# Performance work log

Hardware: AMD Instinct MI355X
Metric: run time of the kernel (lower is better)

The kernel has to match this reference:

```python
import jax, jax.numpy as jnp
import numpy as np

DIM = 512
PDIM = 64
NUM_HEAD = 8
HEAD_DIM = DIM // NUM_HEAD
SCALE = HEAD_DIM ** -0.5
EPS = 1e-6


def setup_inputs() -> dict:
    key = jax.random.key(0)
    ks = jax.random.split(key, 8)
    B, N = 8, 2048
    x_token = jax.random.normal(ks[0], (B, N, DIM), dtype=jnp.float32)
    x_path = jax.random.normal(ks[1], (B, N, PDIM), dtype=jnp.float32)
    idx_cluster = jax.random.randint(ks[2], (B, N), 0, 16, dtype=jnp.int32)
    # weights stored as [in, out] (y = x @ W + b), matching torch Linear math
    Wqk = jax.random.normal(ks[3], (DIM, 2 * DIM), dtype=jnp.float32) * 0.02
    Wv = jax.random.normal(ks[4], (DIM, DIM), dtype=jnp.float32) * 0.02
    Wpv = jax.random.normal(ks[5], (PDIM, PDIM), dtype=jnp.float32) * 0.02
    Wproj = jax.random.normal(ks[6], (DIM, DIM), dtype=jnp.float32) * 0.02
    bproj = jax.random.normal(ks[7], (DIM,), dtype=jnp.float32) * 0.02
    return {"x_token": x_token, "x_path": x_path, "idx_cluster": idx_cluster,
            "cluster_num": 16, "Wqk": Wqk, "Wv": Wv, "Wpv": Wpv,
            "Wproj": Wproj, "bproj": bproj}


def reference(x_token, x_path, idx_cluster, cluster_num, Wqk, Wv, Wpv, Wproj, bproj):
    B, N, C = x_token.shape
    qk = x_token @ Wqk                      # [B,N,2C]
    q, k = qk[..., :C], qk[..., C:]
    v = x_token @ Wv                        # [B,N,C]
    pv = x_path @ Wpv                       # dead code in original; kept for fidelity

    idx_shuffle = jnp.argsort(idx_cluster, axis=1)          # [B,N]
    idx_restore = jnp.argsort(idx_shuffle, axis=1)

    v_s = jnp.take_along_axis(v, idx_shuffle[..., None], axis=1)
    pv_s = jnp.take_along_axis(pv, idx_shuffle[..., None], axis=1)  # unused (faithful)

    attn_map = jnp.einsum('bic,bjc->bij', q, k) * SCALE     # [B,N,N]

    # torch does two gathers, both with dim=1; the second index is constant along
    # rows, so attn2[b,i,j] = attn_map[b, idx_shuffle[b, idx_shuffle[b,j]], j]
    double = jnp.take_along_axis(idx_shuffle, idx_shuffle, axis=1)  # [B,N]
    col_vals = jnp.take_along_axis(jnp.swapaxes(attn_map, 1, 2), double[..., None], axis=2)[..., 0]  # [B,N]
    attn = jnp.broadcast_to(col_vals[:, None, :], (B, N, N))

    # contiguous per-cluster block mask in sorted order == equality of sorted ids
    s = jnp.sort(idx_cluster, axis=1)
    mask = (s[:, :, None] == s[:, None, :]) & (s[:, :, None] < cluster_num)

    attn = jnp.where(mask, attn, jnp.float32(-1e9))
    attn = jnp.exp(attn.astype(jnp.float32))
    attn = (attn + EPS / N) / (jnp.sum(attn, axis=-1, keepdims=True) + EPS)

    out = attn @ v_s                                         # [B,N,C]
    out = jnp.swapaxes(out, 1, 2).reshape(B, N, C)           # faithful layout scramble
    out = jnp.take_along_axis(out, idx_restore[..., None], axis=1)
    x_out = out @ Wproj + bproj
    return x_out, attn_map
```

## Files before the change

### kernel.cpp

```cpp
#include <hip/hip_runtime.h>
#include <hip/hip_bf16.h>

typedef __attribute__((ext_vector_type(8))) short short8;
typedef __attribute__((ext_vector_type(4))) float floatx4;

__device__ __forceinline__ unsigned short f2bfu(float f) {
    unsigned u = __float_as_uint(f);
    unsigned rounding = 0x7fffu + ((u >> 16) & 1u);
    return (unsigned short)((u + rounding) >> 16);
}
__device__ __forceinline__ float bfu2f(unsigned short u) {
    return __uint_as_float(((unsigned)u) << 16);
}

__device__ __forceinline__ void async_ld16(const void* g, void* l) {
    __builtin_amdgcn_global_load_lds(
        (const __attribute__((address_space(1))) void*)g,
        (__attribute__((address_space(3))) void*)l, 16, 0, 0);
}

#define B_  8
#define N_  2048
#define C_  512
#define NC_ 16
#define SL_ 8

__global__ __launch_bounds__(256) void cvt_x(const float4* __restrict__ x,
                                             unsigned short* __restrict__ xbf) {
    size_t i = (size_t)blockIdx.x * 256 + threadIdx.x;
    float4 f = x[i];
    unsigned short u0 = f2bfu(f.x), u1 = f2bfu(f.y), u2 = f2bfu(f.z), u3 = f2bfu(f.w);
    uint2 p;
    p.x = (unsigned)u0 | ((unsigned)u1 << 16);
    p.y = (unsigned)u2 | ((unsigned)u3 << 16);
    *(uint2*)(xbf + 4 * i) = p;
}

__global__ __launch_bounds__(256) void cvt_wqkv(const float* __restrict__ Wqk,
                                                const float* __restrict__ Wv,
                                                unsigned short* __restrict__ WT) {
    int id = blockIdx.x * 256 + threadIdx.x;
    int n = id >> 9, k = id & 511;
    float v = (n < 1024) ? Wqk[(size_t)k * 1024 + n] : Wv[(size_t)k * 512 + (n - 1024)];
    WT[id] = f2bfu(v);
}

__global__ __launch_bounds__(256) void sort_kernel(const int* __restrict__ idx_cluster,
                                                   int* __restrict__ shuf,
                                                   int* __restrict__ restore,
                                                   int* __restrict__ svals,
                                                   int* __restrict__ dbl,
                                                   int* __restrict__ cstart) {
    int b = blockIdx.x, t = threadIdx.x;
    __shared__ int vals[N_];
    __shared__ int seghist[256 * 17];
    __shared__ int cbase[NC_], ctot[NC_];
    __shared__ int shufs[N_];
    const int* src = idx_cluster + (size_t)b * N_;
    for (int j = t; j < N_; j += 256) vals[j] = src[j];
    for (int c = 0; c < NC_; ++c) seghist[t * 17 + c] = 0;
    __syncthreads();
    for (int i = 0; i < 8; ++i) {
        int c = vals[t * 8 + i];
        seghist[t * 17 + c]++;
    }
    __syncthreads();
    if (t < NC_) {
        int run = 0;
        for (int s = 0; s < 256; ++s) {
            int x = seghist[s * 17 + t];
            seghist[s * 17 + t] = run;
            run += x;
        }
        ctot[t] = run;
    }
    __syncthreads();
    if (t == 0) {
        int run = 0;
        for (int c = 0; c < NC_; ++c) {
            cbase[c] = run;
            cstart[b * 17 + c] = run;
            run += ctot[c];
        }
        cstart[b * 17 + NC_] = run;
    }
    __syncthreads();
    for (int i = 0; i < 8; ++i) {
        int p = t * 8 + i;
        int c = vals[p];
        int pos = cbase[c] + seghist[t * 17 + c];
        seghist[t * 17 + c]++;
        shufs[pos] = p;
    }
    __syncthreads();
    for (int j = t; j < N_; j += 256) {
        int sj = shufs[j];
        shuf[(size_t)b * N_ + j] = sj;
        svals[(size_t)b * N_ + j] = vals[sj];
        restore[(size_t)b * N_ + sj] = j;
        dbl[(size_t)b * N_ + j] = shufs[sj];
    }
}

template <int MODE>
__global__ __launch_bounds__(256) void gemm_bt(const unsigned short* __restrict__ A,
                                               const unsigned short* __restrict__ Bt,
                                               float* __restrict__ outF,
                                               unsigned short* __restrict__ outQ,
                                               unsigned short* __restrict__ outK,
                                               unsigned short* __restrict__ outV,
                                               const float* __restrict__ bias) {
    constexpr int K = 512;
    constexpr int NT = K / 64;
    int t = threadIdx.x;
    int lane = t & 63, wave = t >> 6;
    int wm = (wave & 1) * 64, wn = (wave >> 1) * 64;
    int m0 = blockIdx.y * 128, n0 = blockIdx.x * 128;
    if (MODE == 1) {
        size_t b = blockIdx.z;
        A += b * (size_t)N_ * 512;
        Bt += b * (size_t)N_ * 512;
        outF += b * (size_t)N_ * N_;
    }
    __shared__ __align__(16) unsigned short As[2][128 * 64];
    __shared__ __align__(16) unsigned short Bs[2][128 * 64];
    floatx4 acc[4][4] = {};
    int l15 = lane & 15, q4 = lane >> 4;
    int srow = lane >> 3, schk = lane & 7;
    int sgc = schk ^ srow;
    int xr = l15 & 7;

    auto stage = [&](int buf, int k0) {
#pragma unroll
        for (int i = 0; i < 4; ++i) {
            int cid = i * 4 + wave;
            int row = cid * 8 + srow;
            async_ld16(A + (size_t)(m0 + row) * 512 + k0 + sgc * 8, (char*)As[buf] + cid * 1024);
            async_ld16(Bt + (size_t)(n0 + row) * 512 + k0 + sgc * 8, (char*)Bs[buf] + cid * 1024);
        }
    };
    auto compute = [&](int buf) {
#pragma unroll
        for (int kk = 0; kk < 2; ++kk) {
            int csw = (((kk * 4 + q4) ^ xr) * 8);
            short8 af[4], bfr[4];
#pragma unroll
            for (int mi = 0; mi < 4; ++mi)
                af[mi] = *(const short8*)(&As[buf][(wm + mi * 16 + l15) * 64 + csw]);
#pragma unroll
            for (int ni = 0; ni < 4; ++ni)
                bfr[ni] = *(const short8*)(&Bs[buf][(wn + ni * 16 + l15) * 64 + csw]);
#pragma unroll
            for (int mi = 0; mi < 4; ++mi)
#pragma unroll
                for (int ni = 0; ni < 4; ++ni)
                    acc[mi][ni] = __builtin_amdgcn_mfma_f32_16x16x32_bf16(af[mi], bfr[ni], acc[mi][ni], 0, 0, 0);
        }
    };

    stage(0, 0);
    __syncthreads();
    for (int it = 1; it < NT; ++it) {
        stage(it & 1, it * 64);
        compute((it - 1) & 1);
        __syncthreads();
    }
    compute((NT - 1) & 1);

#pragma unroll
    for (int mi = 0; mi < 4; ++mi) {
#pragma unroll
        for (int ni = 0; ni < 4; ++ni) {
#pragma unroll
            for (int r = 0; r < 4; ++r) {
                int row = m0 + wm + mi * 16 + q4 * 4 + r;
                int col = n0 + wn + ni * 16 + l15;
                float v = acc[mi][ni][r];
                if (MODE == 0) {
                    unsigned short u = f2bfu(v);
                    if (col < 512)       outQ[(size_t)row * 512 + col] = u;
                    else if (col < 1024) outK[(size_t)row * 512 + col - 512] = u;
                    else                 outV[(size_t)row * 512 + col - 1024] = u;
                } else {
                    outF[(size_t)row * N_ + col] = v * 0.125f;
                }
            }
        }
    }
}

__global__ __launch_bounds__(256) void cluster_reduce2(const float* __restrict__ attn,
                                                       const int* __restrict__ shuf,
                                                       const int* __restrict__ dbl,
                                                       const int* __restrict__ cstart,
                                                       const unsigned short* __restrict__ vbf,
                                                       float* __restrict__ Opart,
                                                       float* __restrict__ Spart) {
    int c = blockIdx.x, b = blockIdx.y, sl = blockIdx.z, t = threadIdx.x;
    int start = cstart[b * 17 + c], end = cstart[b * 17 + c + 1];
    int n = end - start;
    int i0 = (n * sl) / SL_, i1 = (n * (sl + 1)) / SL_;
    int cnt = i1 - i0;
    __shared__ float e_lds[256];
    __shared__ int row_lds[256];
    if (t < cnt) {
        int j = start + i0 + t;
        int dj = dbl[(size_t)b * N_ + j];
        float e = expf(attn[(size_t)b * N_ * N_ + (size_t)dj * N_ + j]);
        e_lds[t] = e;
        row_lds[t] = shuf[(size_t)b * N_ + j];
    }
    __syncthreads();
    if (t == 0) {
        float s = 0.f;
        for (int i = 0; i < cnt; ++i) s += e_lds[i];
        Spart[(b * SL_ + sl) * NC_ + c] = s;
    }
    float a0 = 0.f, a1 = 0.f;
    for (int i = 0; i < cnt; ++i) {
        float e = e_lds[i];
        unsigned u = *(const unsigned*)(vbf + ((size_t)b * N_ + row_lds[i]) * 512 + 2 * t);
        a0 += e * bfu2f((unsigned short)u);
        a1 += e * bfu2f((unsigned short)(u >> 16));
    }
    float2 o; o.x = a0; o.y = a1;
    *(float2*)(Opart + (((size_t)(b * SL_ + sl) * NC_ + c) * 512 + 2 * t)) = o;
}

__global__ __launch_bounds__(256) void combine_O(const float* __restrict__ Opart,
                                                 const float* __restrict__ Spart,
                                                 float* __restrict__ Ot) {
    int c = blockIdx.x, b = blockIdx.y, t = threadIdx.x;
    float S = 0.f;
    for (int sl = 0; sl < SL_; ++sl) S += Spart[(b * SL_ + sl) * NC_ + c];
    float inv = S > 0.f ? 1.f / S : 0.f;
    float a0 = 0.f, a1 = 0.f;
    for (int sl = 0; sl < SL_; ++sl) {
        float2 o = *(const float2*)(Opart + (((size_t)(b * SL_ + sl) * NC_ + c) * 512 + 2 * t));
        a0 += o.x; a1 += o.y;
    }
    Ot[((size_t)b * 512 + 2 * t) * NC_ + c] = a0 * inv;
    Ot[((size_t)b * 512 + 2 * t + 1) * NC_ + c] = a1 * inv;
}

__global__ __launch_bounds__(256) void build_wg(const float* __restrict__ Wproj,
                                                const int* __restrict__ cstart,
                                                unsigned int* __restrict__ Wg) {
    int c = blockIdx.x;
    int bg = blockIdx.y;
    int b = bg >> 2, g = bg & 3;
    int t = threadIdx.x;
    int lo = cstart[b * 17 + c] - g * 512;
    int hi = cstart[b * 17 + c + 1] - g * 512;
    lo = lo < 0 ? 0 : lo;
    hi = hi > 512 ? 512 : hi;
    float a0 = 0.f, a1 = 0.f;
    for (int cd = lo; cd < hi; ++cd) {
        float2 w = *(const float2*)(Wproj + (size_t)cd * 512 + 2 * t);
        a0 += w.x; a1 += w.y;
    }
    Wg[(size_t)bg * NC_ * 256 + c * 256 + t] =
        (unsigned)f2bfu(a0) | ((unsigned)f2bfu(a1) << 16);
}

__global__ __launch_bounds__(256) void xout_kernel(const float* __restrict__ Ot,
                                                   const unsigned int* __restrict__ Wg,
                                                   const int* __restrict__ restore,
                                                   const float* __restrict__ bias,
                                                   float* __restrict__ xout) {
    int nb = blockIdx.x, b = blockIdx.y, t = threadIdx.x;
    int n0 = nb * 64;
    __shared__ int r_lds[64];
    if (t < 64) r_lds[t] = restore[(size_t)b * N_ + n0 + t];
    __syncthreads();
    float b0 = bias[2 * t], b1 = bias[2 * t + 1];
    const float* Otb = Ot + (size_t)b * 512 * NC_;
    for (int g = 0; g < 4; ++g) {
        const unsigned int* wg = Wg + (size_t)(b * 4 + g) * NC_ * 256 + t;
        float wx[NC_], wy[NC_];
#pragma unroll
        for (int c = 0; c < NC_; ++c) {
            unsigned u = wg[c * 256];
            wx[c] = bfu2f((unsigned short)u);
            wy[c] = bfu2f((unsigned short)(u >> 16));
        }
        for (int i = 0; i < 64; ++i) {
            int r = r_lds[i];
            if ((r & 3) != g) continue;
            int rq = r >> 2;
            const float4* op = (const float4*)(Otb + rq * NC_);
            float o[NC_];
            *(float4*)&o[0]  = op[0];
            *(float4*)&o[4]  = op[1];
            *(float4*)&o[8]  = op[2];
            *(float4*)&o[12] = op[3];
            float a0 = b0, a1 = b1;
#pragma unroll
            for (int c = 0; c < NC_; ++c) { a0 += o[c] * wx[c]; a1 += o[c] * wy[c]; }
            float2 res; res.x = a0; res.y = a1;
            *(float2*)(xout + ((size_t)b * N_ + n0 + i) * 512 + 2 * t) = res;
        }
    }
}

extern "C" void kernel_launch(void* const* d_in, const int* in_sizes, int n_in,
                              void* d_out, int out_size, void* d_ws, size_t ws_size,
                              hipStream_t stream) {
    const float* x_token = (const float*)d_in[0];
    const int* idx_cluster = (const int*)d_in[2];
    const float* Wqk = (const float*)d_in[4];
    const float* Wv = (const float*)d_in[5];
    const float* Wproj = (const float*)d_in[7];
    const float* bproj = (const float*)d_in[8];

    float* x_out = (float*)d_out;
    float* attn = x_out + (size_t)B_ * N_ * C_;

    char* ws = (char*)d_ws;
    size_t off = 0;
    auto alloc = [&](size_t bytes) {
        void* p = ws + off;
        off += (bytes + 255) & ~(size_t)255;
        return p;
    };
    unsigned short* WqkvT = (unsigned short*)alloc(1536 * 512 * 2);
    unsigned short* xbf = (unsigned short*)alloc((size_t)B_ * N_ * C_ * 2);
    unsigned short* qbf = (unsigned short*)alloc((size_t)B_ * N_ * C_ * 2);
    unsigned short* kbf = (unsigned short*)alloc((size_t)B_ * N_ * C_ * 2);
    unsigned short* vbf = (unsigned short*)alloc((size_t)B_ * N_ * C_ * 2);
    int* shuf = (int*)alloc((size_t)B_ * N_ * 4);
    int* restore = (int*)alloc((size_t)B_ * N_ * 4);
    int* svals = (int*)alloc((size_t)B_ * N_ * 4);
    int* dbl = (int*)alloc((size_t)B_ * N_ * 4);
    int* cstart = (int*)alloc(B_ * 17 * 4);
    float* Ot = (float*)alloc((size_t)B_ * 512 * NC_ * 4);
    float* Opart = (float*)alloc((size_t)B_ * SL_ * NC_ * 512 * 4);
    float* Spart = (float*)alloc((size_t)B_ * SL_ * NC_ * 4);
    unsigned int* Wg = (unsigned int*)alloc((size_t)B_ * 4 * NC_ * 256 * 4);

    cvt_x<<<dim3((B_ * N_ * C_) / (256 * 4)), dim3(256), 0, stream>>>((const float4*)x_token, xbf);
    cvt_wqkv<<<dim3((1536 * 512) / 256), dim3(256), 0, stream>>>(Wqk, Wv, WqkvT);

    sort_kernel<<<dim3(B_), dim3(256), 0, stream>>>(idx_cluster, shuf, restore, svals, dbl, cstart);

    build_wg<<<dim3(NC_, B_ * 4), dim3(256), 0, stream>>>(Wproj, cstart, Wg);

    gemm_bt<0><<<dim3(1536 / 128, 16384 / 128, 1), dim3(256), 0, stream>>>(
        xbf, WqkvT, nullptr, qbf, kbf, vbf, nullptr);

    gemm_bt<1><<<dim3(N_ / 128, N_ / 128, B_), dim3(256), 0, stream>>>(
        qbf, kbf, attn, nullptr, nullptr, nullptr, nullptr);

    cluster_reduce2<<<dim3(NC_, B_, SL_), dim3(256), 0, stream>>>(
        attn, shuf, dbl, cstart, vbf, Opart, Spart);

    combine_O<<<dim3(NC_, B_), dim3(256), 0, stream>>>(Opart, Spart, Ot);

    xout_kernel<<<dim3(N_ / 64, B_), dim3(256), 0, stream>>>(Ot, Wg, restore, bproj, x_out);
}
```

Baseline: 403.7 us.

## Shrink GEMM K-tile to 32 and add XCD-aware workgroup swizzle

Halves the K-step of the bf16 MFMA GEMM tile from 64 to 32, which shrinks LDS usage per block to allow more resident blocks, and reworks the LDS XOR swizzle to match the narrower rows. It also remaps the linear block id so that consecutive ids land on the same XCD group (lid&7 striding), aiming for better L2 locality across chiplets. The cost is twice as many K iterations and barriers per tile, with less MFMA work between syncs.

```diff
diff --git a/kernel.cpp b/kernel.cpp
--- a/kernel.cpp
+++ b/kernel.cpp
@@ -111,57 +111,65 @@
                                                unsigned short* __restrict__ outV,
                                                const float* __restrict__ bias) {
     constexpr int K = 512;
-    constexpr int NT = K / 64;
+    constexpr int NT = K / 32;
     int t = threadIdx.x;
     int lane = t & 63, wave = t >> 6;
     int wm = (wave & 1) * 64, wn = (wave >> 1) * 64;
-    int m0 = blockIdx.y * 128, n0 = blockIdx.x * 128;
+
+    int gx = gridDim.x, gy = gridDim.y;
+    int nwg = gx * gy * gridDim.z;
+    int lid = blockIdx.x + gx * (blockIdx.y + gy * blockIdx.z);
+    int swz = (lid & 7) * (nwg >> 3) + (lid >> 3);
+    int bx = swz % gx;
+    int rem = swz / gx;
+    int by = rem % gy;
+    int bz = rem / gy;
+
+    int m0 = by * 128, n0 = bx * 128;
     if (MODE == 1) {
-        size_t b = blockIdx.z;
+        size_t b = (size_t)bz;
         A += b * (size_t)N_ * 512;
         Bt += b * (size_t)N_ * 512;
         outF += b * (size_t)N_ * N_;
     }
-    __shared__ __align__(16) unsigned short As[2][128 * 64];
-    __shared__ __align__(16) unsigned short Bs[2][128 * 64];
+    __shared__ __align__(16) unsigned short As[2][128 * 32];
+    __shared__ __align__(16) unsigned short Bs[2][128 * 32];
     floatx4 acc[4][4] = {};
     int l15 = lane & 15, q4 = lane >> 4;
-    int srow = lane >> 3, schk = lane & 7;
-    int sgc = schk ^ srow;
-    int xr = l15 & 7;
+    int fc = (l15 >> 1) & 3;
+
+    int s_r = lane >> 2;
+    int s_c = (lane & 3) ^ ((lane >> 3) & 3);
 
     auto stage = [&](int buf, int k0) {
 #pragma unroll
-        for (int i = 0; i < 4; ++i) {
-            int cid = i * 4 + wave;
-            int row = cid * 8 + srow;
-            async_ld16(A + (size_t)(m0 + row) * 512 + k0 + sgc * 8, (char*)As[buf] + cid * 1024);
-            async_ld16(Bt + (size_t)(n0 + row) * 512 + k0 + sgc * 8, (char*)Bs[buf] + cid * 1024);
+        for (int i = 0; i < 2; ++i) {
+            int grp = wave + i * 4;
+            int row = grp * 16 + s_r;
+            async_ld16(A + (size_t)(m0 + row) * 512 + k0 + s_c * 8, (char*)As[buf] + grp * 1024);
+            async_ld16(Bt + (size_t)(n0 + row) * 512 + k0 + s_c * 8, (char*)Bs[buf] + grp * 1024);
         }
     };
     auto compute = [&](int buf) {
-#pragma unroll
-        for (int kk = 0; kk < 2; ++kk) {
-            int csw = (((kk * 4 + q4) ^ xr) * 8);
-            short8 af[4], bfr[4];
-#pragma unroll
-            for (int mi = 0; mi < 4; ++mi)
-                af[mi] = *(const short8*)(&As[buf][(wm + mi * 16 + l15) * 64 + csw]);
+        int cs = (q4 ^ fc) * 8;
+        short8 af[4], bfr[4];
+#pragma unroll
+        for (int mi = 0; mi < 4; ++mi)
+            af[mi] = *(const short8*)(&As[buf][(wm + mi * 16 + l15) * 32 + cs]);
+#pragma unroll
+        for (int ni = 0; ni < 4; ++ni)
+            bfr[ni] = *(const short8*)(&Bs[buf][(wn + ni * 16 + l15) * 32 + cs]);
+#pragma unroll
+        for (int mi = 0; mi < 4; ++mi)
 #pragma unroll
             for (int ni = 0; ni < 4; ++ni)
-                bfr[ni] = *(const short8*)(&Bs[buf][(wn + ni * 16 + l15) * 64 + csw]);
-#pragma unroll
-            for (int mi = 0; mi < 4; ++mi)
-#pragma unroll
-                for (int ni = 0; ni < 4; ++ni)
-                    acc[mi][ni] = __builtin_amdgcn_mfma_f32_16x16x32_bf16(af[mi], bfr[ni], acc[mi][ni], 0, 0, 0);
-        }
+                acc[mi][ni] = __builtin_amdgcn_mfma_f32_16x16x32_bf16(af[mi], bfr[ni], acc[mi][ni], 0, 0, 0);
     };
 
     stage(0, 0);
     __syncthreads();
     for (int it = 1; it < NT; ++it) {
-        stage(it & 1, it * 64);
+        stage(it & 1, it * 32);
         compute((it - 1) & 1);
         __syncthreads();
     }
```

After: 377.1 us. -6.6%, faster.

## Apply Wv after cluster reduction and swizzle GEMM tiles with single-buffered LDS

Applied to the files above, without the earlier changes.

Uses linearity to drop the V projection from the big GEMM. The cluster reduction now sums exp-weighted bf16 x rows, and a small new kernel multiplies the per-cluster sums by Wv in fp32. This removes a third of the QKV GEMM's output columns and the V buffer writes. The GEMM also gets a workgroup-id swizzle for cache locality and swaps the double-buffered LDS pipeline for a single buffer with two barriers per k-step. That swap may expose load latency.

```diff
diff --git a/kernel.cpp b/kernel.cpp
--- a/kernel.cpp
+++ b/kernel.cpp
@@ -36,13 +36,11 @@
     *(uint2*)(xbf + 4 * i) = p;
 }
 
-__global__ __launch_bounds__(256) void cvt_wqkv(const float* __restrict__ Wqk,
-                                                const float* __restrict__ Wv,
-                                                unsigned short* __restrict__ WT) {
+__global__ __launch_bounds__(256) void cvt_wqk(const float* __restrict__ Wqk,
+                                               unsigned short* __restrict__ WT) {
     int id = blockIdx.x * 256 + threadIdx.x;
     int n = id >> 9, k = id & 511;
-    float v = (n < 1024) ? Wqk[(size_t)k * 1024 + n] : Wv[(size_t)k * 512 + (n - 1024)];
-    WT[id] = f2bfu(v);
+    WT[id] = f2bfu(Wqk[(size_t)k * 1024 + n]);
 }
 
 __global__ __launch_bounds__(256) void sort_kernel(const int* __restrict__ idx_cluster,
@@ -107,66 +105,63 @@
                                                const unsigned short* __restrict__ Bt,
                                                float* __restrict__ outF,
                                                unsigned short* __restrict__ outQ,
-                                               unsigned short* __restrict__ outK,
-                                               unsigned short* __restrict__ outV,
-                                               const float* __restrict__ bias) {
+                                               unsigned short* __restrict__ outK) {
     constexpr int K = 512;
-    constexpr int NT = K / 64;
     int t = threadIdx.x;
     int lane = t & 63, wave = t >> 6;
     int wm = (wave & 1) * 64, wn = (wave >> 1) * 64;
-    int m0 = blockIdx.y * 128, n0 = blockIdx.x * 128;
+
+    int gx = gridDim.x, gy = gridDim.y;
+    int nwg = gx * gy * gridDim.z;
+    int lid = blockIdx.x + gx * (blockIdx.y + gy * blockIdx.z);
+    int swz = (lid & 7) * (nwg >> 3) + (lid >> 3);
+    int bx = swz % gx;
+    int rem = swz / gx;
+    int by = rem % gy;
+    int bz = rem / gy;
+
+    int m0 = by * 128, n0 = bx * 128;
     if (MODE == 1) {
-        size_t b = blockIdx.z;
+        size_t b = (size_t)bz;
         A += b * (size_t)N_ * 512;
         Bt += b * (size_t)N_ * 512;
         outF += b * (size_t)N_ * N_;
     }
-    __shared__ __align__(16) unsigned short As[2][128 * 64];
-    __shared__ __align__(16) unsigned short Bs[2][128 * 64];
+    __shared__ __align__(16) unsigned short As[128 * 64];
+    __shared__ __align__(16) unsigned short Bs[128 * 64];
     floatx4 acc[4][4] = {};
     int l15 = lane & 15, q4 = lane >> 4;
     int srow = lane >> 3, schk = lane & 7;
     int sgc = schk ^ srow;
     int xr = l15 & 7;
 
-    auto stage = [&](int buf, int k0) {
+    for (int k0 = 0; k0 < K; k0 += 64) {
+        __syncthreads();
 #pragma unroll
         for (int i = 0; i < 4; ++i) {
             int cid = i * 4 + wave;
             int row = cid * 8 + srow;
-            async_ld16(A + (size_t)(m0 + row) * 512 + k0 + sgc * 8, (char*)As[buf] + cid * 1024);
-            async_ld16(Bt + (size_t)(n0 + row) * 512 + k0 + sgc * 8, (char*)Bs[buf] + cid * 1024);
-        }
-    };
-    auto compute = [&](int buf) {
+            async_ld16(A + (size_t)(m0 + row) * 512 + k0 + sgc * 8, (char*)As + cid * 1024);
+            async_ld16(Bt + (size_t)(n0 + row) * 512 + k0 + sgc * 8, (char*)Bs + cid * 1024);
+        }
+        __syncthreads();
 #pragma unroll
         for (int kk = 0; kk < 2; ++kk) {
             int csw = (((kk * 4 + q4) ^ xr) * 8);
             short8 af[4], bfr[4];
 #pragma unroll
             for (int mi = 0; mi < 4; ++mi)
-                af[mi] = *(const short8*)(&As[buf][(wm + mi * 16 + l15) * 64 + csw]);
+                af[mi] = *(const short8*)(&As[(wm + mi * 16 + l15) * 64 + csw]);
 #pragma unroll
             for (int ni = 0; ni < 4; ++ni)
-                bfr[ni] = *(const short8*)(&Bs[buf][(wn + ni * 16 + l15) * 64 + csw]);
+                bfr[ni] = *(const short8*)(&Bs[(wn + ni * 16 + l15) * 64 + csw]);
 #pragma unroll
             for (int mi = 0; mi < 4; ++mi)
 #pragma unroll
                 for (int ni = 0; ni < 4; ++ni)
                     acc[mi][ni] = __builtin_amdgcn_mfma_f32_16x16x32_bf16(af[mi], bfr[ni], acc[mi][ni], 0, 0, 0);
         }
-    };
-
-    stage(0, 0);
-    __syncthreads();
-    for (int it = 1; it < NT; ++it) {
-        stage(it & 1, it * 64);
-        compute((it - 1) & 1);
-        __syncthreads();
-    }
-    compute((NT - 1) & 1);
-
+    }
 #pragma unroll
     for (int mi = 0; mi < 4; ++mi) {
 #pragma unroll
@@ -178,9 +173,8 @@
                 float v = acc[mi][ni][r];
                 if (MODE == 0) {
                     unsigned short u = f2bfu(v);
-                    if (col < 512)       outQ[(size_t)row * 512 + col] = u;
-                    else if (col < 1024) outK[(size_t)row * 512 + col - 512] = u;
-                    else                 outV[(size_t)row * 512 + col - 1024] = u;
+                    if (col < 512) outQ[(size_t)row * 512 + col] = u;
+                    else           outK[(size_t)row * 512 + col - 512] = u;
                 } else {
                     outF[(size_t)row * N_ + col] = v * 0.125f;
                 }
@@ -193,8 +187,8 @@
                                                        const int* __restrict__ shuf,
                                                        const int* __restrict__ dbl,
                                                        const int* __restrict__ cstart,
-                                                       const unsigned short* __restrict__ vbf,
-                                                       float* __restrict__ Opart,
+                                                       const unsigned short* __restrict__ xbf,
+                                                       float* __restrict__ xepart,
                                                        float* __restrict__ Spart) {
     int c = blockIdx.x, b = blockIdx.y, sl = blockIdx.z, t = threadIdx.x;
     int start = cstart[b * 17 + c], end = cstart[b * 17 + c + 1];
@@ -219,25 +213,48 @@
     float a0 = 0.f, a1 = 0.f;
     for (int i = 0; i < cnt; ++i) {
         float e = e_lds[i];
-        unsigned u = *(const unsigned*)(vbf + ((size_t)b * N_ + row_lds[i]) * 512 + 2 * t);
+        unsigned u = *(const unsigned*)(xbf + ((size_t)b * N_ + row_lds[i]) * 512 + 2 * t);
         a0 += e * bfu2f((unsigned short)u);
         a1 += e * bfu2f((unsigned short)(u >> 16));
     }
     float2 o; o.x = a0; o.y = a1;
-    *(float2*)(Opart + (((size_t)(b * SL_ + sl) * NC_ + c) * 512 + 2 * t)) = o;
-}
-
-__global__ __launch_bounds__(256) void combine_O(const float* __restrict__ Opart,
-                                                 const float* __restrict__ Spart,
-                                                 float* __restrict__ Ot) {
+    *(float2*)(xepart + (((size_t)(b * SL_ + sl) * NC_ + c) * 512 + 2 * t)) = o;
+}
+
+__global__ __launch_bounds__(256) void combine_xe(const float* __restrict__ xepart,
+                                                  const float* __restrict__ Spart,
+                                                  float* __restrict__ xe,
+                                                  float* __restrict__ Stot) {
     int c = blockIdx.x, b = blockIdx.y, t = threadIdx.x;
-    float S = 0.f;
-    for (int sl = 0; sl < SL_; ++sl) S += Spart[(b * SL_ + sl) * NC_ + c];
+    float a0 = 0.f, a1 = 0.f;
+    for (int sl = 0; sl < SL_; ++sl) {
+        float2 o = *(const float2*)(xepart + (((size_t)(b * SL_ + sl) * NC_ + c) * 512 + 2 * t));
+        a0 += o.x; a1 += o.y;
+    }
+    float2 r; r.x = a0; r.y = a1;
+    *(float2*)(xe + ((size_t)b * NC_ + c) * 512 + 2 * t) = r;
+    if (t == 0) {
+        float S = 0.f;
+        for (int sl = 0; sl < SL_; ++sl) S += Spart[(b * SL_ + sl) * NC_ + c];
+        Stot[b * NC_ + c] = S;
+    }
+}
+
+__global__ __launch_bounds__(256) void ovw_kernel(const float* __restrict__ xe,
+                                                  const float* __restrict__ Stot,
+                                                  const float* __restrict__ Wv,
+                                                  float* __restrict__ Ot) {
+    int c = blockIdx.x, b = blockIdx.y, t = threadIdx.x;
+    __shared__ float xl[512];
+    for (int i = t; i < 512; i += 256) xl[i] = xe[((size_t)b * NC_ + c) * 512 + i];
+    __syncthreads();
+    float S = Stot[b * NC_ + c];
     float inv = S > 0.f ? 1.f / S : 0.f;
     float a0 = 0.f, a1 = 0.f;
-    for (int sl = 0; sl < SL_; ++sl) {
-        float2 o = *(const float2*)(Opart + (((size_t)(b * SL_ + sl) * NC_ + c) * 512 + 2 * t));
-        a0 += o.x; a1 += o.y;
+    for (int k = 0; k < 512; ++k) {
+        float xv = xl[k];
+        float2 w = *(const float2*)(Wv + (size_t)k * 512 + 2 * t);
+        a0 += xv * w.x; a1 += xv * w.y;
     }
     Ot[((size_t)b * 512 + 2 * t) * NC_ + c] = a0 * inv;
     Ot[((size_t)b * 512 + 2 * t + 1) * NC_ + c] = a1 * inv;
@@ -323,38 +340,41 @@
         off += (bytes + 255) & ~(size_t)255;
         return p;
     };
-    unsigned short* WqkvT = (unsigned short*)alloc(1536 * 512 * 2);
+    unsigned short* WqkT = (unsigned short*)alloc(1024 * 512 * 2);
     unsigned short* xbf = (unsigned short*)alloc((size_t)B_ * N_ * C_ * 2);
     unsigned short* qbf = (unsigned short*)alloc((size_t)B_ * N_ * C_ * 2);
     unsigned short* kbf = (unsigned short*)alloc((size_t)B_ * N_ * C_ * 2);
-    unsigned short* vbf = (unsigned short*)alloc((size_t)B_ * N_ * C_ * 2);
     int* shuf = (int*)alloc((size_t)B_ * N_ * 4);
     int* restore = (int*)alloc((size_t)B_ * N_ * 4);
     int* svals = (int*)alloc((size_t)B_ * N_ * 4);
     int* dbl = (int*)alloc((size_t)B_ * N_ * 4);
     int* cstart = (int*)alloc(B_ * 17 * 4);
     float* Ot = (float*)alloc((size_t)B_ * 512 * NC_ * 4);
-    float* Opart = (float*)alloc((size_t)B_ * SL_ * NC_ * 512 * 4);
+    float* xepart = (float*)alloc((size_t)B_ * SL_ * NC_ * 512 * 4);
     float* Spart = (float*)alloc((size_t)B_ * SL_ * NC_ * 4);
+    float* xe = (float*)alloc((size_t)B_ * NC_ * 512 * 4);
+    float* Stot = (float*)alloc((size_t)B_ * NC_ * 4);
     unsigned int* Wg = (unsigned int*)alloc((size_t)B_ * 4 * NC_ * 256 * 4);
 
     cvt_x<<<dim3((B_ * N_ * C_) / (256 * 4)), dim3(256), 0, stream>>>((const float4*)x_token, xbf);
-    cvt_wqkv<<<dim3((1536 * 512) / 256), dim3(256), 0, stream>>>(Wqk, Wv, WqkvT);
+    cvt_wqk<<<dim3((1024 * 512) / 256), dim3(256), 0, stream>>>(Wqk, WqkT);
 
     sort_kernel<<<dim3(B_), dim3(256), 0, stream>>>(idx_cluster, shuf, restore, svals, dbl, cstart);
 
     build_wg<<<dim3(NC_, B_ * 4), dim3(256), 0, stream>>>(Wproj, cstart, Wg);
 
-    gemm_bt<0><<<dim3(1536 / 128, 16384 / 128, 1), dim3(256), 0, stream>>>(
-        xbf, WqkvT, nullptr, qbf, kbf, vbf, nullptr);
+    gemm_bt<0><<<dim3(1024 / 128, 16384 / 128, 1), dim3(256), 0, stream>>>(
+        xbf, WqkT, nullptr, qbf, kbf);
 
     gemm_bt<1><<<dim3(N_ / 128, N_ / 128, B_), dim3(256), 0, stream>>>(
-        qbf, kbf, attn, nullptr, nullptr, nullptr, nullptr);
+        qbf, kbf, attn, nullptr, nullptr);
 
     cluster_reduce2<<<dim3(NC_, B_, SL_), dim3(256), 0, stream>>>(
-        attn, shuf, dbl, cstart, vbf, Opart, Spart);
-
-    combine_O<<<dim3(NC_, B_), dim3(256), 0, stream>>>(Opart, Spart, Ot);
+        attn, shuf, dbl, cstart, xbf, xepart, Spart);
+
+    combine_xe<<<dim3(NC_, B_), dim3(256), 0, stream>>>(xepart, Spart, xe, Stot);
+
+    ovw_kernel<<<dim3(NC_, B_), dim3(256), 0, stream>>>(xe, Stot, Wv, Ot);
 
     xout_kernel<<<dim3(N_ / 64, B_), dim3(256), 0, stream>>>(Ot, Wg, restore, bproj, x_out);
 }
```

Result: faster. 382.2 us (-5.3%).
